# Kernel optimization log

Hardware: AMD Instinct MI355X
Metric: run time of the kernel (lower is better)

## Reference

```python
import jax, jax.numpy as jnp
import numpy as np

B, L, C = 4, 16384, 512   # batch, tokens (128x128 grid), dim
NH, WS = 8, 8             # num_heads, window grid (ws)
HD = C // NH              # head_dim = 64


def setup_inputs() -> dict:
    key = jax.random.key(0)
    k1, k2, k3, k4, k5 = jax.random.split(key, 5)
    return {
        "q":   jax.random.normal(k1, (B, L, C), dtype=jnp.float32),
        "kv":  jax.random.normal(k2, (B, L, C), dtype=jnp.float32),
        "Wq":  jax.random.normal(k3, (C, C), dtype=jnp.float32) * 0.02,
        "Wkv": jax.random.normal(k4, (C, 2 * C), dtype=jnp.float32) * 0.02,
        "Wfc": jax.random.normal(k5, (C, C), dtype=jnp.float32) * 0.02,
    }


def reference(q, kv, Wq, Wkv, Wfc):
    Bq, Lq, Cd = q.shape
    Lkv = kv.shape[1]
    nh, hd, ws = NH, Cd // NH, WS
    scale = hd ** (-0.5)
    hw_q = int(round(Lq ** 0.5))   # 128
    hw_k = int(round(Lkv ** 0.5))
    sq, sk = hw_q // ws, hw_k // ws  # window side lengths (16)

    qp = q @ Wq                                   # [B, Lq, C]
    kvp = (kv @ Wkv).reshape(Bq, Lkv, 2, Cd)
    k, v = kvp[:, :, 0], kvp[:, :, 1]             # [B, Lkv, C]

    def window(x, s):
        # [B, hw, hw, C] -> [B, ws*ws windows, heads, s*s tokens, hd]
        x = x.reshape(Bq, ws, s, ws, s, Cd).transpose(0, 1, 3, 2, 4, 5)
        x = x.reshape(Bq, ws * ws, s * s, nh, hd)
        return x.transpose(0, 1, 3, 2, 4)

    qw = window(qp, sq)   # [B, W, H, sq*sq, hd]
    kw = window(k, sk)    # [B, W, H, sk*sk, hd]
    vw = window(v, sk)

    attn = jnp.einsum('bwhqd,bwhkd->bwhqk', qw, kw) * scale
    attn = jax.nn.softmax(attn, axis=-1)
    o = jnp.einsum('bwhqk,bwhkd->bwhqd', attn, vw)  # [B, W, H, sq*sq, hd]

    # inverse window partition
    o = o.transpose(0, 1, 3, 2, 4).reshape(Bq, ws, ws, sq, sq, Cd)
    o = o.transpose(0, 1, 3, 2, 4, 5).reshape(Bq, Lq, Cd)
    return o @ Wfc
```

## Files before the change

kernel.cpp:

```cpp
#include <hip/hip_runtime.h>
#include <stdint.h>

#define BB 4
#define LL 16384
#define CC 512
#define MM (BB * LL)

typedef unsigned short u16;
typedef __bf16 bf16x8 __attribute__((ext_vector_type(8)));
typedef float f32x4 __attribute__((ext_vector_type(4)));
typedef u16 u16x8 __attribute__((ext_vector_type(8)));
typedef u16 u16x4 __attribute__((ext_vector_type(4)));

__device__ __forceinline__ u16 f2bf(float f) {
  return __builtin_bit_cast(u16, (__bf16)f);
}

__device__ __forceinline__ void gl_lds16(const void* g, void* l) {
  __builtin_amdgcn_global_load_lds((const __attribute__((address_space(1))) void*)g,
                                   (__attribute__((address_space(3))) void*)l,
                                   16, 0, 0);
}

__global__ __launch_bounds__(256) void prep_kernel(
    const float* __restrict__ q, const float* __restrict__ kv,
    const float* __restrict__ Wq, const float* __restrict__ Wkv,
    const float* __restrict__ Wfc, u16* __restrict__ qo, u16* __restrict__ kvo,
    u16* __restrict__ Wq_t, u16* __restrict__ Wkv_t, u16* __restrict__ Wfc_t) {
  __shared__ float tile[64][65];
  const int bid = blockIdx.x, tid = threadIdx.x;

  if (bid < 4096) {
    const int half = bid >> 11;
    const float* src = half ? kv : q;
    u16* dst = half ? kvo : qo;
    const int n16 = MM * CC / 16;
    const int stride = 2048 * 256;
    for (int i = (bid & 2047) * 256 + tid; i < n16; i += stride) {
      const f32x4* sp = reinterpret_cast<const f32x4*>(src) + 4 * i;
      f32x4 a0 = __builtin_nontemporal_load(sp + 0);
      f32x4 a1 = __builtin_nontemporal_load(sp + 1);
      f32x4 a2 = __builtin_nontemporal_load(sp + 2);
      f32x4 a3 = __builtin_nontemporal_load(sp + 3);
      u16x8 o0, o1;
      o0[0] = f2bf(a0[0]); o0[1] = f2bf(a0[1]); o0[2] = f2bf(a0[2]); o0[3] = f2bf(a0[3]);
      o0[4] = f2bf(a1[0]); o0[5] = f2bf(a1[1]); o0[6] = f2bf(a1[2]); o0[7] = f2bf(a1[3]);
      o1[0] = f2bf(a2[0]); o1[1] = f2bf(a2[1]); o1[2] = f2bf(a2[2]); o1[3] = f2bf(a2[3]);
      o1[4] = f2bf(a3[0]); o1[5] = f2bf(a3[1]); o1[6] = f2bf(a3[2]); o1[7] = f2bf(a3[3]);
      reinterpret_cast<u16x8*>(dst)[2 * i + 0] = o0;
      reinterpret_cast<u16x8*>(dst)[2 * i + 1] = o1;
    }
    return;
  }

  const int wb = bid - 4096;
  const float* W; u16* Wt; int N, ti;
  if (wb < 64)       { W = Wq;  Wt = Wq_t;  N = 512;  ti = wb; }
  else if (wb < 192) { W = Wkv; Wt = Wkv_t; N = 1024; ti = wb - 64; }
  else               { W = Wfc; Wt = Wfc_t; N = 512;  ti = wb - 192; }
  const int ntn = N >> 6;
  const int kt = ti / ntn, nt = ti % ntn;
  const int k0 = kt << 6, n0 = nt << 6;
  {
    const int r = tid >> 4, c4 = tid & 15;
#pragma unroll
    for (int e = 0; e < 4; ++e) {
      int row = r + e * 16;
      f32x4 v = *reinterpret_cast<const f32x4*>(&W[(size_t)(k0 + row) * N + n0 + c4 * 4]);
      tile[row][c4 * 4 + 0] = v[0]; tile[row][c4 * 4 + 1] = v[1];
      tile[row][c4 * 4 + 2] = v[2]; tile[row][c4 * 4 + 3] = v[3];
    }
  }
  __syncthreads();
  {
    const int n = tid >> 2, qd = tid & 3;
#pragma unroll
    for (int e = 0; e < 2; ++e) {
      int c = qd * 2 + e;
      u16x8 o;
#pragma unroll
      for (int j = 0; j < 8; ++j) o[j] = f2bf(tile[c * 8 + j][n]);
      *reinterpret_cast<u16x8*>(&Wt[(size_t)(n0 + n) * 512 + k0 + c * 8]) = o;
    }
  }
}

template <bool OUT_F32>
__global__ __launch_bounds__(256, 3) void gemm128(const u16* __restrict__ A,
                                                  const u16* __restrict__ Bt,
                                                  void* __restrict__ Cp,
                                                  int N, int nbnl) {
  constexpr int K = 512;
  constexpr int NT = 8;
  __shared__ __align__(16) u16 Al[2][8192];
  __shared__ __align__(16) u16 Bl[8192];
  const int nwg = gridDim.x;
  const int bid0 = blockIdx.x;
  const int cpx = nwg >> 3;
  const int bid = (bid0 & 7) * cpx + (bid0 >> 3);
  const int bm = bid >> nbnl, bn = bid & ((1 << nbnl) - 1);
  const size_t row0 = (size_t)bm << 7, col0 = (size_t)bn << 7;
  const int tid = threadIdx.x, lane = tid & 63;
  const int wv = tid >> 6, wm = wv >> 1, wn = wv & 1;
  const int ro = lane & 15, g4 = lane >> 4;

  auto stageA = [&](int kt, u16* L) {
#pragma unroll
    for (int c = 0; c < 4; ++c) {
      int cc = tid + c * 256;
      int r = cc >> 3, g = (cc & 7) ^ (r & 7);
      gl_lds16(A + (row0 + r) * (size_t)K + kt * 64 + g * 8, L + cc * 8);
    }
  };
  auto stageB = [&](int kt) {
#pragma unroll
    for (int c = 0; c < 4; ++c) {
      int cc = tid + c * 256;
      int r = cc >> 3, g = (cc & 7) ^ (r & 7);
      gl_lds16(Bt + (col0 + r) * (size_t)K + kt * 64 + g * 8, Bl + cc * 8);
    }
  };

  const int aB = (wm * 64 + ro) * 64;
  const int bB = (wn * 64 + ro) * 64;
  const int sw0 = (g4 ^ (ro & 7)) * 8;
  const int sw1 = ((g4 + 4) ^ (ro & 7)) * 8;

  auto ldf = [&](const u16* p) { return *reinterpret_cast<const bf16x8*>(p); };

  f32x4 acc[4][4] = {};

  stageA(0, Al[0]); stageB(0);
  asm volatile("s_waitcnt vmcnt(0)" ::: "memory");
  __builtin_amdgcn_s_barrier();

  for (int u = 0; u < NT; ++u) {
    u16* LA = Al[u & 1];
    u16* LAn = Al[(u + 1) & 1];
    const bool st = (u + 1) < NT;
    bf16x8 bfr[4][2], af[2][2];

#pragma unroll
    for (int n = 0; n < 4; ++n) {
      bfr[n][0] = ldf(Bl + bB + n * 1024 + sw0);
      bfr[n][1] = ldf(Bl + bB + n * 1024 + sw1);
    }
    af[0][0] = ldf(LA + aB + sw0);        af[0][1] = ldf(LA + aB + sw1);
    af[1][0] = ldf(LA + aB + 1024 + sw0); af[1][1] = ldf(LA + aB + 1024 + sw1);
    if (st) stageA(u + 1, LAn);
    __builtin_amdgcn_s_barrier();
    asm volatile("s_waitcnt lgkmcnt(0)" ::: "memory");
    __builtin_amdgcn_sched_barrier(0);
    __builtin_amdgcn_s_setprio(1);
#pragma unroll
    for (int m = 0; m < 2; ++m)
#pragma unroll
      for (int n = 0; n < 4; ++n) {
        acc[m][n] = __builtin_amdgcn_mfma_f32_16x16x32_bf16(af[m][0], bfr[n][0], acc[m][n], 0, 0, 0);
        acc[m][n] = __builtin_amdgcn_mfma_f32_16x16x32_bf16(af[m][1], bfr[n][1], acc[m][n], 0, 0, 0);
      }
    __builtin_amdgcn_s_setprio(0);
    __builtin_amdgcn_s_barrier();

    af[0][0] = ldf(LA + aB + 2048 + sw0); af[0][1] = ldf(LA + aB + 2048 + sw1);
    af[1][0] = ldf(LA + aB + 3072 + sw0); af[1][1] = ldf(LA + aB + 3072 + sw1);
    if (st) stageB(u + 1);
    __builtin_amdgcn_s_barrier();
    asm volatile("s_waitcnt lgkmcnt(0)" ::: "memory");
    __builtin_amdgcn_sched_barrier(0);
    __builtin_amdgcn_s_setprio(1);
#pragma unroll
    for (int m = 0; m < 2; ++m)
#pragma unroll
      for (int n = 0; n < 4; ++n) {
        acc[2 + m][n] = __builtin_amdgcn_mfma_f32_16x16x32_bf16(af[m][0], bfr[n][0], acc[2 + m][n], 0, 0, 0);
        acc[2 + m][n] = __builtin_amdgcn_mfma_f32_16x16x32_bf16(af[m][1], bfr[n][1], acc[2 + m][n], 0, 0, 0);
      }
    __builtin_amdgcn_s_setprio(0);
    asm volatile("s_waitcnt vmcnt(0)" ::: "memory");
    __builtin_amdgcn_s_barrier();
  }

#pragma unroll
  for (int m = 0; m < 4; ++m)
#pragma unroll
    for (int n = 0; n < 4; ++n)
#pragma unroll
      for (int j = 0; j < 4; ++j) {
        size_t r = row0 + wm * 64 + m * 16 + g4 * 4 + j;
        size_t c = col0 + wn * 64 + n * 16 + ro;
        if (OUT_F32)
          reinterpret_cast<float*>(Cp)[r * N + c] = acc[m][n][j];
        else
          reinterpret_cast<u16*>(Cp)[r * N + c] = f2bf(acc[m][n][j]);
      }
}

__global__ __launch_bounds__(512, 4) void attn_kernel(const u16* __restrict__ qp,
                                                      const u16* __restrict__ kvp,
                                                      u16* __restrict__ o) {
  __shared__ __align__(16) u16 Kl[256 * 64];
  __shared__ __align__(16) u16 Vt[64 * 256];
  __shared__ __align__(16) u16 Pl[8 * 1024];
  const int bid = blockIdx.x;
  const int h = bid & 7, w = (bid >> 3) & 63, b = bid >> 9;
  const int w1 = w >> 3, w2 = w & 7;
  const int tid = threadIdx.x, lane = tid & 63, wv = tid >> 6;

  auto lrow = [&](int t) { return (w1 * 16 + (t >> 4)) * 128 + w2 * 16 + (t & 15); };

#pragma unroll
  for (int p = 0; p < 4; ++p) {
    int ci = tid + p * 512;
    int r = ci >> 3, g = (ci & 7) ^ (r & 7);
    gl_lds16(kvp + ((size_t)(b * LL + lrow(r))) * 1024 + h * 64 + g * 8, Kl + ci * 8);
  }
  {
    const int tk = tid >> 1, half = tid & 1;
    const size_t base = ((size_t)(b * LL + lrow(tk))) * 1024 + 512 + h * 64 + half * 32;
#pragma unroll
    for (int c = 0; c < 4; ++c) {
      u16x8 vx = *reinterpret_cast<const u16x8*>(kvp + base + c * 8);
#pragma unroll
      for (int e = 0; e < 8; ++e) {
        int d = half * 32 + c * 8 + e;
        Vt[d * 256 + (((tk >> 3) ^ (d & 7)) * 8) + (tk & 7)] = vx[e];
      }
    }
  }
  __syncthreads();

  const int ro = lane & 15;
  const int g4 = lane >> 4;
  const float scale = 0.125f;
  const int swA = (g4 ^ (ro & 7)) * 8;
  const int swB = ((g4 + 4) ^ (ro & 7)) * 8;
  u16* PW = Pl + wv * 1024;

  auto ldf = [&](const u16* p) { return *reinterpret_cast<const bf16x8*>(p); };

#pragma unroll
  for (int rt = 0; rt < 2; ++rt) {
    const int tq = 32 * wv + 16 * rt + ro;
    const size_t qbase = ((size_t)(b * LL + lrow(tq))) * 512 + h * 64 + g4 * 8;
    const bf16x8 qf0 = *reinterpret_cast<const bf16x8*>(qp + qbase);
    const bf16x8 qf1 = *reinterpret_cast<const bf16x8*>(qp + qbase + 32);

    f32x4 sa[16] = {};
    __builtin_amdgcn_s_setprio(1);
#pragma unroll
    for (int ct = 0; ct < 16; ++ct) {
      bf16x8 kf0 = ldf(Kl + (16 * ct + ro) * 64 + swA);
      bf16x8 kf1 = ldf(Kl + (16 * ct + ro) * 64 + swB);
      sa[ct] = __builtin_amdgcn_mfma_f32_16x16x32_bf16(qf0, kf0, sa[ct], 0, 0, 0);
      sa[ct] = __builtin_amdgcn_mfma_f32_16x16x32_bf16(qf1, kf1, sa[ct], 0, 0, 0);
    }
    __builtin_amdgcn_s_setprio(0);

#pragma unroll
    for (int j = 0; j < 4; ++j) {
      float m = -1e30f;
#pragma unroll
      for (int ct = 0; ct < 16; ++ct) m = fmaxf(m, sa[ct][j]);
      m = fmaxf(m, __shfl_xor(m, 1));
      m = fmaxf(m, __shfl_xor(m, 2));
      m = fmaxf(m, __shfl_xor(m, 4));
      m = fmaxf(m, __shfl_xor(m, 8));
      m *= scale;
      float s = 0.f;
#pragma unroll
      for (int ct = 0; ct < 16; ++ct) {
        float p = __expf(sa[ct][j] * scale - m);
        sa[ct][j] = p;
        s += p;
      }
      s += __shfl_xor(s, 1);
      s += __shfl_xor(s, 2);
      s += __shfl_xor(s, 4);
      s += __shfl_xor(s, 8);
      float inv = 1.f / s;
#pragma unroll
      for (int ct = 0; ct < 16; ++ct) sa[ct][j] *= inv;
    }

    f32x4 oacc[4] = {};
#pragma unroll
    for (int kh = 0; kh < 4; ++kh) {
#pragma unroll
      for (int c = 0; c < 4; ++c)
#pragma unroll
        for (int j = 0; j < 4; ++j) {
          int rq = g4 * 4 + j;
          PW[rq * 64 + (((2 * c + (ro >> 3)) ^ (rq & 7)) * 8) + (ro & 7)] =
              f2bf(sa[kh * 4 + c][j]);
        }
      __builtin_amdgcn_s_setprio(1);
#pragma unroll
      for (int ks = 0; ks < 2; ++ks) {
        bf16x8 pf = ldf(PW + ro * 64 + (((ks * 4 + g4) ^ (ro & 7)) * 8));
        const int kkg = kh * 2 + ks;
#pragma unroll
        for (int cd = 0; cd < 4; ++cd) {
          bf16x8 vf = ldf(Vt + (16 * cd + ro) * 256 + (((kkg * 4 + g4) ^ (ro & 7)) * 8));
          oacc[cd] = __builtin_amdgcn_mfma_f32_16x16x32_bf16(pf, vf, oacc[cd], 0, 0, 0);
        }
      }
      __builtin_amdgcn_s_setprio(0);
    }

#pragma unroll
    for (int cd = 0; cd < 4; ++cd)
#pragma unroll
      for (int j = 0; j < 4; ++j) {
        int t = 32 * wv + 16 * rt + g4 * 4 + j;
        int d = 16 * cd + ro;
        o[((size_t)(b * LL + lrow(t))) * 512 + h * 64 + d] = f2bf(oacc[cd][j]);
      }
  }
}

extern "C" void kernel_launch(void* const* d_in, const int* in_sizes, int n_in,
                              void* d_out, int out_size, void* d_ws, size_t ws_size,
                              hipStream_t stream) {
  const float* q = (const float*)d_in[0];
  const float* kv = (const float*)d_in[1];
  const float* Wq = (const float*)d_in[2];
  const float* Wkv = (const float*)d_in[3];
  const float* Wfc = (const float*)d_in[4];
  float* out = (float*)d_out;
  char* ws = (char*)d_ws;

  u16* q_bf  = (u16*)(ws + 0);
  u16* kv_bf = (u16*)(ws + 67108864);
  u16* qp    = (u16*)(ws + 134217728);
  u16* kvp   = (u16*)(ws + 201326592);
  u16* Wq_t  = (u16*)(ws + 335544320);
  u16* Wkv_t = (u16*)(ws + 336068608);
  u16* Wfc_t = (u16*)(ws + 337117184);
  u16* o_buf = q_bf;

  prep_kernel<<<4352, 256, 0, stream>>>(q, kv, Wq, Wkv, Wfc, q_bf, kv_bf, Wq_t, Wkv_t, Wfc_t);

  gemm128<false><<<2048, 256, 0, stream>>>(q_bf, Wq_t, qp, CC, 2);
  gemm128<false><<<4096, 256, 0, stream>>>(kv_bf, Wkv_t, kvp, 2 * CC, 3);

  attn_kernel<<<BB * 64 * 8, 512, 0, stream>>>(qp, kvp, o_buf);

  gemm128<true><<<2048, 256, 0, stream>>>(o_buf, Wfc_t, out, CC, 2);
}
```

Baseline: 366.7 us.

## Enlarge GEMM tiles to 256x128, restructure prep, V transpose, and softmax

The GEMM moves to 256x128 tiles with 512 threads and 8 waves. Its inner loop is re-pipelined into four MFMA phases, using partial lgkmcnt waits and fewer barriers, to get more reuse of B per block. The fp32-to-bf16 conversion now has each block issue 16 coalesced loads up front instead of a grid-stride loop. The attention kernel writes the V transpose as paired u16x2 stores, uses exp2 with a prescaled log2e factor, and defers the softmax normalization to the output. These changes touch several kernels at once, and the bigger tiles raise LDS and register pressure, which may lower occupancy.

```diff
diff --git a/kernel.cpp b/kernel.cpp
--- a/kernel.cpp
+++ b/kernel.cpp
@@ -11,6 +11,7 @@
 typedef float f32x4 __attribute__((ext_vector_type(4)));
 typedef u16 u16x8 __attribute__((ext_vector_type(8)));
 typedef u16 u16x4 __attribute__((ext_vector_type(4)));
+typedef u16 u16x2 __attribute__((ext_vector_type(2)));
 
 __device__ __forceinline__ u16 f2bf(float f) {
   return __builtin_bit_cast(u16, (__bf16)f);
@@ -34,21 +35,23 @@
     const int half = bid >> 11;
     const float* src = half ? kv : q;
     u16* dst = half ? kvo : qo;
-    const int n16 = MM * CC / 16;
-    const int stride = 2048 * 256;
-    for (int i = (bid & 2047) * 256 + tid; i < n16; i += stride) {
-      const f32x4* sp = reinterpret_cast<const f32x4*>(src) + 4 * i;
-      f32x4 a0 = __builtin_nontemporal_load(sp + 0);
-      f32x4 a1 = __builtin_nontemporal_load(sp + 1);
-      f32x4 a2 = __builtin_nontemporal_load(sp + 2);
-      f32x4 a3 = __builtin_nontemporal_load(sp + 3);
-      u16x8 o0, o1;
-      o0[0] = f2bf(a0[0]); o0[1] = f2bf(a0[1]); o0[2] = f2bf(a0[2]); o0[3] = f2bf(a0[3]);
-      o0[4] = f2bf(a1[0]); o0[5] = f2bf(a1[1]); o0[6] = f2bf(a1[2]); o0[7] = f2bf(a1[3]);
-      o1[0] = f2bf(a2[0]); o1[1] = f2bf(a2[1]); o1[2] = f2bf(a2[2]); o1[3] = f2bf(a2[3]);
-      o1[4] = f2bf(a3[0]); o1[5] = f2bf(a3[1]); o1[6] = f2bf(a3[2]); o1[7] = f2bf(a3[3]);
-      reinterpret_cast<u16x8*>(dst)[2 * i + 0] = o0;
-      reinterpret_cast<u16x8*>(dst)[2 * i + 1] = o1;
+    const int lb = bid & 2047;
+    const int c0 = lb * 4096;
+    f32x4 v[16];
+#pragma unroll
+    for (int k = 0; k < 16; ++k)
+      v[k] = __builtin_nontemporal_load(reinterpret_cast<const f32x4*>(src) + c0 + k * 256 + tid);
+#pragma unroll
+    for (int k = 0; k < 8; ++k) {
+      u16x8 o;
+#pragma unroll
+      for (int e = 0; e < 4; ++e) o[e] = f2bf(v[2 * k][e]);
+#pragma unroll
+      for (int e = 0; e < 4; ++e) o[4 + e] = f2bf(v[2 * k + 1][e]);
+      *reinterpret_cast<u16x4*>(dst + (size_t)(c0 + 2 * k * 256 + tid) * 4) =
+          (u16x4){o[0], o[1], o[2], o[3]};
+      *reinterpret_cast<u16x4*>(dst + (size_t)(c0 + (2 * k + 1) * 256 + tid) * 4) =
+          (u16x4){o[4], o[5], o[6], o[7]};
     }
     return;
   }
@@ -86,20 +89,20 @@
 }
 
 template <bool OUT_F32>
-__global__ __launch_bounds__(256, 3) void gemm128(const u16* __restrict__ A,
+__global__ __launch_bounds__(512, 4) void gemm256(const u16* __restrict__ A,
                                                   const u16* __restrict__ Bt,
                                                   void* __restrict__ Cp,
                                                   int N, int nbnl) {
   constexpr int K = 512;
   constexpr int NT = 8;
-  __shared__ __align__(16) u16 Al[2][8192];
+  __shared__ __align__(16) u16 Al[2][16384];
   __shared__ __align__(16) u16 Bl[8192];
   const int nwg = gridDim.x;
   const int bid0 = blockIdx.x;
   const int cpx = nwg >> 3;
   const int bid = (bid0 & 7) * cpx + (bid0 >> 3);
   const int bm = bid >> nbnl, bn = bid & ((1 << nbnl) - 1);
-  const size_t row0 = (size_t)bm << 7, col0 = (size_t)bn << 7;
+  const size_t row0 = (size_t)bm << 8, col0 = (size_t)bn << 7;
   const int tid = threadIdx.x, lane = tid & 63;
   const int wv = tid >> 6, wm = wv >> 1, wn = wv & 1;
   const int ro = lane & 15, g4 = lane >> 4;
@@ -107,15 +110,15 @@
   auto stageA = [&](int kt, u16* L) {
 #pragma unroll
     for (int c = 0; c < 4; ++c) {
-      int cc = tid + c * 256;
+      int cc = tid + c * 512;
       int r = cc >> 3, g = (cc & 7) ^ (r & 7);
       gl_lds16(A + (row0 + r) * (size_t)K + kt * 64 + g * 8, L + cc * 8);
     }
   };
   auto stageB = [&](int kt) {
 #pragma unroll
-    for (int c = 0; c < 4; ++c) {
-      int cc = tid + c * 256;
+    for (int c = 0; c < 2; ++c) {
+      int cc = tid + c * 512;
       int r = cc >> 3, g = (cc & 7) ^ (r & 7);
       gl_lds16(Bt + (col0 + r) * (size_t)K + kt * 64 + g * 8, Bl + cc * 8);
     }
@@ -138,44 +141,59 @@
     u16* LA = Al[u & 1];
     u16* LAn = Al[(u + 1) & 1];
     const bool st = (u + 1) < NT;
-    bf16x8 bfr[4][2], af[2][2];
+    bf16x8 bfr[4][2], afa[2], afb[2];
 
 #pragma unroll
     for (int n = 0; n < 4; ++n) {
       bfr[n][0] = ldf(Bl + bB + n * 1024 + sw0);
       bfr[n][1] = ldf(Bl + bB + n * 1024 + sw1);
     }
-    af[0][0] = ldf(LA + aB + sw0);        af[0][1] = ldf(LA + aB + sw1);
-    af[1][0] = ldf(LA + aB + 1024 + sw0); af[1][1] = ldf(LA + aB + 1024 + sw1);
+    afa[0] = ldf(LA + aB + sw0); afa[1] = ldf(LA + aB + sw1);
     if (st) stageA(u + 1, LAn);
+    asm volatile("s_waitcnt lgkmcnt(0)" ::: "memory");
+    __builtin_amdgcn_sched_barrier(0);
+    afb[0] = ldf(LA + aB + 1024 + sw0); afb[1] = ldf(LA + aB + 1024 + sw1);
+    __builtin_amdgcn_sched_barrier(0);
+    __builtin_amdgcn_s_setprio(1);
+#pragma unroll
+    for (int n = 0; n < 4; ++n) {
+      acc[0][n] = __builtin_amdgcn_mfma_f32_16x16x32_bf16(afa[0], bfr[n][0], acc[0][n], 0, 0, 0);
+      acc[0][n] = __builtin_amdgcn_mfma_f32_16x16x32_bf16(afa[1], bfr[n][1], acc[0][n], 0, 0, 0);
+    }
+    __builtin_amdgcn_s_setprio(0);
     __builtin_amdgcn_s_barrier();
+
+    if (st) stageB(u + 1);
+    afa[0] = ldf(LA + aB + 2048 + sw0); afa[1] = ldf(LA + aB + 2048 + sw1);
+    asm volatile("s_waitcnt lgkmcnt(2)" ::: "memory");
+    __builtin_amdgcn_sched_barrier(0);
+    __builtin_amdgcn_s_setprio(1);
+#pragma unroll
+    for (int n = 0; n < 4; ++n) {
+      acc[1][n] = __builtin_amdgcn_mfma_f32_16x16x32_bf16(afb[0], bfr[n][0], acc[1][n], 0, 0, 0);
+      acc[1][n] = __builtin_amdgcn_mfma_f32_16x16x32_bf16(afb[1], bfr[n][1], acc[1][n], 0, 0, 0);
+    }
+    __builtin_amdgcn_s_setprio(0);
+
+    afb[0] = ldf(LA + aB + 3072 + sw0); afb[1] = ldf(LA + aB + 3072 + sw1);
+    asm volatile("s_waitcnt lgkmcnt(2)" ::: "memory");
+    __builtin_amdgcn_sched_barrier(0);
+    __builtin_amdgcn_s_setprio(1);
+#pragma unroll
+    for (int n = 0; n < 4; ++n) {
+      acc[2][n] = __builtin_amdgcn_mfma_f32_16x16x32_bf16(afa[0], bfr[n][0], acc[2][n], 0, 0, 0);
+      acc[2][n] = __builtin_amdgcn_mfma_f32_16x16x32_bf16(afa[1], bfr[n][1], acc[2][n], 0, 0, 0);
+    }
+    __builtin_amdgcn_s_setprio(0);
+
     asm volatile("s_waitcnt lgkmcnt(0)" ::: "memory");
     __builtin_amdgcn_sched_barrier(0);
     __builtin_amdgcn_s_setprio(1);
 #pragma unroll
-    for (int m = 0; m < 2; ++m)
-#pragma unroll
-      for (int n = 0; n < 4; ++n) {
-        acc[m][n] = __builtin_amdgcn_mfma_f32_16x16x32_bf16(af[m][0], bfr[n][0], acc[m][n], 0, 0, 0);
-        acc[m][n] = __builtin_amdgcn_mfma_f32_16x16x32_bf16(af[m][1], bfr[n][1], acc[m][n], 0, 0, 0);
-      }
-    __builtin_amdgcn_s_setprio(0);
-    __builtin_amdgcn_s_barrier();
-
-    af[0][0] = ldf(LA + aB + 2048 + sw0); af[0][1] = ldf(LA + aB + 2048 + sw1);
-    af[1][0] = ldf(LA + aB + 3072 + sw0); af[1][1] = ldf(LA + aB + 3072 + sw1);
-    if (st) stageB(u + 1);
-    __builtin_amdgcn_s_barrier();
-    asm volatile("s_waitcnt lgkmcnt(0)" ::: "memory");
-    __builtin_amdgcn_sched_barrier(0);
-    __builtin_amdgcn_s_setprio(1);
-#pragma unroll
-    for (int m = 0; m < 2; ++m)
-#pragma unroll
-      for (int n = 0; n < 4; ++n) {
-        acc[2 + m][n] = __builtin_amdgcn_mfma_f32_16x16x32_bf16(af[m][0], bfr[n][0], acc[2 + m][n], 0, 0, 0);
-        acc[2 + m][n] = __builtin_amdgcn_mfma_f32_16x16x32_bf16(af[m][1], bfr[n][1], acc[2 + m][n], 0, 0, 0);
-      }
+    for (int n = 0; n < 4; ++n) {
+      acc[3][n] = __builtin_amdgcn_mfma_f32_16x16x32_bf16(afb[0], bfr[n][0], acc[3][n], 0, 0, 0);
+      acc[3][n] = __builtin_amdgcn_mfma_f32_16x16x32_bf16(afb[1], bfr[n][1], acc[3][n], 0, 0, 0);
+    }
     __builtin_amdgcn_s_setprio(0);
     asm volatile("s_waitcnt vmcnt(0)" ::: "memory");
     __builtin_amdgcn_s_barrier();
@@ -216,23 +234,33 @@
     gl_lds16(kvp + ((size_t)(b * LL + lrow(r))) * 1024 + h * 64 + g * 8, Kl + ci * 8);
   }
   {
-    const int tk = tid >> 1, half = tid & 1;
-    const size_t base = ((size_t)(b * LL + lrow(tk))) * 1024 + 512 + h * 64 + half * 32;
-#pragma unroll
-    for (int c = 0; c < 4; ++c) {
-      u16x8 vx = *reinterpret_cast<const u16x8*>(kvp + base + c * 8);
-#pragma unroll
-      for (int e = 0; e < 8; ++e) {
-        int d = half * 32 + c * 8 + e;
-        Vt[d * 256 + (((tk >> 3) ^ (d & 7)) * 8) + (tk & 7)] = vx[e];
-      }
+    const int pr = tid >> 2;
+    const int dg = tid & 3;
+    const int t0 = 2 * pr;
+    const size_t b0 = ((size_t)(b * LL + lrow(t0))) * 1024 + 512 + h * 64 + dg * 16;
+    const size_t b1 = ((size_t)(b * LL + lrow(t0 + 1))) * 1024 + 512 + h * 64 + dg * 16;
+    u16x8 v00 = *reinterpret_cast<const u16x8*>(kvp + b0);
+    u16x8 v01 = *reinterpret_cast<const u16x8*>(kvp + b0 + 8);
+    u16x8 v10 = *reinterpret_cast<const u16x8*>(kvp + b1);
+    u16x8 v11 = *reinterpret_cast<const u16x8*>(kvp + b1 + 8);
+#pragma unroll
+    for (int e = 0; e < 8; ++e) {
+      int d = dg * 16 + e;
+      *reinterpret_cast<u16x2*>(
+          &Vt[d * 256 + (((t0 >> 3) ^ (d & 7)) * 8) + (t0 & 7)]) = (u16x2){v00[e], v10[e]};
+    }
+#pragma unroll
+    for (int e = 0; e < 8; ++e) {
+      int d = dg * 16 + 8 + e;
+      *reinterpret_cast<u16x2*>(
+          &Vt[d * 256 + (((t0 >> 3) ^ (d & 7)) * 8) + (t0 & 7)]) = (u16x2){v01[e], v11[e]};
     }
   }
   __syncthreads();
 
   const int ro = lane & 15;
   const int g4 = lane >> 4;
-  const float scale = 0.125f;
+  const float kk = 0.125f * 1.44269504f;
   const int swA = (g4 ^ (ro & 7)) * 8;
   const int swB = ((g4 + 4) ^ (ro & 7)) * 8;
   u16* PW = Pl + wv * 1024;
@@ -257,20 +285,24 @@
     }
     __builtin_amdgcn_s_setprio(0);
 
+    float inv4[4];
 #pragma unroll
     for (int j = 0; j < 4; ++j) {
-      float m = -1e30f;
-#pragma unroll
-      for (int ct = 0; ct < 16; ++ct) m = fmaxf(m, sa[ct][j]);
+      float t8[8];
+#pragma unroll
+      for (int i = 0; i < 8; ++i) t8[i] = fmaxf(sa[i][j], sa[i + 8][j]);
+      float t4a = fmaxf(t8[0], t8[1]), t4b = fmaxf(t8[2], t8[3]);
+      float t4c = fmaxf(t8[4], t8[5]), t4d = fmaxf(t8[6], t8[7]);
+      float m = fmaxf(fmaxf(t4a, t4b), fmaxf(t4c, t4d));
       m = fmaxf(m, __shfl_xor(m, 1));
       m = fmaxf(m, __shfl_xor(m, 2));
       m = fmaxf(m, __shfl_xor(m, 4));
       m = fmaxf(m, __shfl_xor(m, 8));
-      m *= scale;
+      const float mk = m * kk;
       float s = 0.f;
 #pragma unroll
       for (int ct = 0; ct < 16; ++ct) {
-        float p = __expf(sa[ct][j] * scale - m);
+        float p = exp2f(sa[ct][j] * kk - mk);
         sa[ct][j] = p;
         s += p;
       }
@@ -278,9 +310,7 @@
       s += __shfl_xor(s, 2);
       s += __shfl_xor(s, 4);
       s += __shfl_xor(s, 8);
-      float inv = 1.f / s;
-#pragma unroll
-      for (int ct = 0; ct < 16; ++ct) sa[ct][j] *= inv;
+      inv4[j] = 1.f / s;
     }
 
     f32x4 oacc[4] = {};
@@ -314,7 +344,7 @@
       for (int j = 0; j < 4; ++j) {
         int t = 32 * wv + 16 * rt + g4 * 4 + j;
         int d = 16 * cd + ro;
-        o[((size_t)(b * LL + lrow(t))) * 512 + h * 64 + d] = f2bf(oacc[cd][j]);
+        o[((size_t)(b * LL + lrow(t))) * 512 + h * 64 + d] = f2bf(oacc[cd][j] * inv4[j]);
       }
   }
 }
@@ -341,10 +371,10 @@
 
   prep_kernel<<<4352, 256, 0, stream>>>(q, kv, Wq, Wkv, Wfc, q_bf, kv_bf, Wq_t, Wkv_t, Wfc_t);
 
-  gemm128<false><<<2048, 256, 0, stream>>>(q_bf, Wq_t, qp, CC, 2);
-  gemm128<false><<<4096, 256, 0, stream>>>(kv_bf, Wkv_t, kvp, 2 * CC, 3);
+  gemm256<false><<<(MM / 256) * (CC / 128), 512, 0, stream>>>(q_bf, Wq_t, qp, CC, 2);
+  gemm256<false><<<(MM / 256) * (2 * CC / 128), 512, 0, stream>>>(kv_bf, Wkv_t, kvp, 2 * CC, 3);
 
   attn_kernel<<<BB * 64 * 8, 512, 0, stream>>>(qp, kvp, o_buf);
 
-  gemm128<true><<<2048, 256, 0, stream>>>(o_buf, Wfc_t, out, CC, 2);
-}
+  gemm256<true><<<(MM / 256) * (CC / 128), 512, 0, stream>>>(o_buf, Wfc_t, out, CC, 2);
+}
```

Result: slower. 388.1 us (+5.8%).
